# Optimization experiments

Measured on AMD Instinct MI355X. Metric: run time of the kernel, lower is better.

Reference implementation:

```python
import jax, jax.numpy as jnp
import numpy as np

TEMPERATURE = 0.5
TAU_PLUS = 0.1
EPS = 1e-8


def setup_inputs() -> dict:
    key = jax.random.key(0)
    k1, k2 = jax.random.split(key)
    B, D = 8192, 128
    z_i = jax.random.normal(k1, (B, D), dtype=jnp.float32)
    z_j = jax.random.normal(k2, (B, D), dtype=jnp.float32)
    return {"z_i": z_i, "z_j": z_j}


def _l2_normalize(x, axis=1, eps=1e-12):
    # matches torch F.normalize: x / max(||x||, eps)
    n = jnp.linalg.norm(x, axis=axis, keepdims=True)
    return x / jnp.maximum(n, eps)


def reference(z_i, z_j):
    B = z_i.shape[0]
    zi = _l2_normalize(z_i, axis=1)
    zj = _l2_normalize(z_j, axis=1)
    reps = jnp.concatenate([zi, zj], axis=0)  # [2B, D]
    sim = jnp.matmul(reps, reps.T) / TEMPERATURE  # [2B, 2B]
    sim = sim - jnp.max(sim, axis=1, keepdims=True)
    mask = jnp.eye(2 * B, dtype=bool)
    sim = jnp.where(mask, -9e15, sim)
    pos = jnp.exp(jnp.sum(zi * zj, axis=-1) / TEMPERATURE)  # [B]
    positives = jnp.concatenate([pos, pos], axis=0)  # [2B]
    neg_sum = jnp.sum(jnp.exp(sim), axis=1)  # [2B]
    Ng = (-TAU_PLUS * B * positives + neg_sum) / (1.0 - TAU_PLUS)
    Ng = jnp.maximum(Ng, B * jnp.exp(jnp.asarray(-1.0 / TEMPERATURE, dtype=sim.dtype)))
    loss = -jnp.log(positives / (positives + Ng + EPS))
    return jnp.mean(loss)
```

## Files before the change

### kernel.cpp

```cpp
#include <hip/hip_runtime.h>
#include <hip/hip_bf16.h>

typedef __attribute__((ext_vector_type(8))) short bf16x8;
typedef __attribute__((ext_vector_type(4))) float f32x4;

#define B_ROWS 8192
#define NROWS 16384
#define D 128
#define C1 2.8853900817779268f
#define E_M2 0.13533528323661270f
#define RSCALE 1.6986436f
#define TILE_COLS 64
#define TILE_BYTES (TILE_COLS * D * 2)
#define NSPLIT 16
#define NBLK (64 * NSPLIT)
#define NSLICE 8

__device__ __forceinline__ float fast_exp2(float x) {
#if __has_builtin(__builtin_amdgcn_exp2f)
    return __builtin_amdgcn_exp2f(x);
#else
    float r; asm("v_exp_f32 %0, %1" : "=v"(r) : "v"(x)); return r;
#endif
}
__device__ __forceinline__ float fast_log2(float x) {
#if __has_builtin(__builtin_amdgcn_logf)
    return __builtin_amdgcn_logf(x);
#else
    float r; asm("v_log_f32 %0, %1" : "=v"(r) : "v"(x)); return r;
#endif
}

__device__ __forceinline__ unsigned short f2bf(float f) {
    union { float f; unsigned u; } v; v.f = f;
    unsigned r = v.u + 0x7FFFu + ((v.u >> 16) & 1u);
    return (unsigned short)(r >> 16);
}

__device__ __host__ __forceinline__ int colpart_off(int I) {
    return I * NROWS - 128 * I * (I + 1);
}

__global__ __launch_bounds__(256) void k_norm(const float* __restrict__ zi,
                                              const float* __restrict__ zj,
                                              unsigned* __restrict__ repsU,
                                              float* __restrict__ pos) {
    int w = threadIdx.x >> 6, lane = threadIdx.x & 63;
    int row = blockIdx.x * 4 + w;
    const float2* a2 = (const float2*)(zi + (size_t)row * D);
    const float2* b2 = (const float2*)(zj + (size_t)row * D);
    float2 a = a2[lane], b = b2[lane];
    float si = a.x * a.x + a.y * a.y;
    float sj = b.x * b.x + b.y * b.y;
    float sd = a.x * b.x + a.y * b.y;
#pragma unroll
    for (int m = 32; m; m >>= 1) {
        si += __shfl_xor(si, m);
        sj += __shfl_xor(sj, m);
        sd += __shfl_xor(sd, m);
    }
    float inv_i = 1.0f / fmaxf(sqrtf(si), 1e-12f);
    float inv_j = 1.0f / fmaxf(sqrtf(sj), 1e-12f);
    float sa = inv_i * RSCALE, sb = inv_j * RSCALE;
    repsU[(size_t)row * 64 + lane] =
        (unsigned)f2bf(a.x * sa) | ((unsigned)f2bf(a.y * sa) << 16);
    repsU[(size_t)(row + B_ROWS) * 64 + lane] =
        (unsigned)f2bf(b.x * sb) | ((unsigned)f2bf(b.y * sb) << 16);
    if (lane == 0) pos[row] = fast_exp2(sd * inv_i * inv_j * C1);
}

__global__ __launch_bounds__(256, 2) void k_negsum(const unsigned short* __restrict__ R,
                                                   float* __restrict__ rowpart,
                                                   float* __restrict__ colpart) {
    __shared__ char smem[2][TILE_BYTES];
    __shared__ float colacc[2][4][4][80];
    int I = blockIdx.x >> 4;
    int s = blockIdx.x & (NSPLIT - 1);
    int rowBase = I << 8;
    int dph = (s - ((I << 2) & 15)) & 15;
    int jstart = (I << 2) + dph;
    int nt = (jstart < 256) ? (((255 - jstart) >> 4) + 1) : 0;

    int w = threadIdx.x >> 6;
    int lane = threadIdx.x & 63;
    int lr = lane & 15, lk = lane >> 4;
    int waveRow = rowBase + w * 64;

    bf16x8 afrag[4][4];
#pragma unroll
    for (int r = 0; r < 4; ++r)
#pragma unroll
        for (int kk = 0; kk < 4; ++kk)
            afrag[r][kk] = *(const bf16x8*)(R + (size_t)(waveRow + r * 16 + lr) * D + kk * 32 + lk * 8);

    int srcoff[4], dstoff[4];
#pragma unroll
    for (int j = 0; j < 4; ++j) {
        int o = (w * 4 + j) * 1024 + lane * 16;
        int row = o >> 8, c = o & 255;
        srcoff[j] = row * 256 + (c ^ ((row & 7) << 4));
        dstoff[j] = (w * 4 + j) * 1024;
    }

    const char* Rb = (const char*)R;

    int m64 = (lr & 4) << 4;
    int lbase = lr * 256 + ((lk * 16) ^ ((lr & 3) << 4));

    float acc[4][4] = {};

#define STAGE(buf, jj)                                                            \
    do {                                                                          \
        const char* tb_ = Rb + (size_t)(jj) * (TILE_COLS * 256);                  \
        _Pragma("unroll")                                                         \
        for (int j = 0; j < 4; ++j)                                               \
            __builtin_amdgcn_global_load_lds(                                     \
                (const __attribute__((address_space(1))) unsigned*)(tb_ + srcoff[j]), \
                (__attribute__((address_space(3))) unsigned*)(&smem[buf][dstoff[j]]), \
                16, 0, 0);                                                        \
    } while (0)

#define BATCH_BODY(DIAG)                                                          \
    do {                                                                          \
        _Pragma("unroll")                                                         \
        for (int ct = 0; ct < 4; ++ct) {                                          \
            _Pragma("unroll")                                                     \
            for (int r = 0; r < 4; ++r) {                                         \
                f32x4 c = {0.f, 0.f, 0.f, 0.f};                                   \
                c = __builtin_amdgcn_mfma_f32_16x16x32_bf16(afrag[r][0], bf[ct][0], c, 0, 0, 0); \
                c = __builtin_amdgcn_mfma_f32_16x16x32_bf16(afrag[r][1], bf[ct][1], c, 0, 0, 0); \
                c = __builtin_amdgcn_mfma_f32_16x16x32_bf16(afrag[r][2], bf[ct][2], c, 0, 0, 0); \
                c = __builtin_amdgcn_mfma_f32_16x16x32_bf16(afrag[r][3], bf[ct][3], c, 0, 0, 0); \
                if (DIAG && ct == r) {                                            \
                    _Pragma("unroll")                                             \
                    for (int q = 0; q < 4; ++q)                                   \
                        if (lk * 4 + q != lr) {                                   \
                            float e = fast_exp2(c[q]);                            \
                            acc[r][q] += e; csum[ct] += e;                        \
                        }                                                         \
                } else {                                                          \
                    _Pragma("unroll")                                             \
                    for (int q = 0; q < 4; ++q) {                                 \
                        float e = fast_exp2(c[q]);                                \
                        acc[r][q] += e; csum[ct] += e;                            \
                    }                                                             \
                }                                                                 \
            }                                                                     \
        }                                                                         \
    } while (0)

    if (nt > 0) STAGE(0, jstart);
    __syncthreads();
    int cur = 0;
    for (int t = 0; t < nt; ++t) {
        int jt = jstart + (t << 4);
        int colBase = jt << 6;
        if (t > 0 && w == ((t + 3) & 3)) {
            int pcb = colBase - 1024;
            if (pcb >= rowBase + 256) {
                int par = (t - 1) & 1;
                float v = 0.f;
#pragma unroll
                for (int u = 0; u < 16; ++u) v += colacc[par][u >> 2][u & 3][lane];
                colpart[colpart_off(I) + pcb + lane - ((I + 1) << 8)] = v;
            }
        }
        if (t + 1 < nt) STAGE(cur ^ 1, jt + 16);
        const char* sb = &smem[cur][0] + lbase;
        bf16x8 bf[4][4];
#pragma unroll
        for (int ct = 0; ct < 4; ++ct)
#pragma unroll
            for (int kk = 0; kk < 4; ++kk)
                bf[ct][kk] = *(const bf16x8*)(sb + ct * 4096 + ((kk * 64) ^ m64));
        float csum[4] = {0.f, 0.f, 0.f, 0.f};
        bool offdiag = (colBase >= rowBase + 256);
        if (colBase == waveRow) {
            BATCH_BODY(true);
        } else {
            BATCH_BODY(false);
        }
        if (offdiag) {
            int par = t & 1;
#pragma unroll
            for (int ct = 0; ct < 4; ++ct)
                colacc[par][w][lk][ct * 16 + lr] = csum[ct];
        }
        __syncthreads();
        cur ^= 1;
    }
    if (nt > 0 && w == ((nt + 3) & 3)) {
        int pcb = (jstart + ((nt - 1) << 4)) << 6;
        if (pcb >= rowBase + 256) {
            int par = (nt - 1) & 1;
            float v = 0.f;
#pragma unroll
            for (int u = 0; u < 16; ++u) v += colacc[par][u >> 2][u & 3][lane];
            colpart[colpart_off(I) + pcb + lane - ((I + 1) << 8)] = v;
        }
    }
#undef STAGE
#undef BATCH_BODY

#pragma unroll
    for (int r = 0; r < 4; ++r)
#pragma unroll
        for (int q = 0; q < 4; ++q) {
            float v = acc[r][q];
            v += __shfl_xor(v, 1);
            v += __shfl_xor(v, 2);
            v += __shfl_xor(v, 4);
            v += __shfl_xor(v, 8);
            if (lr == 0)
                rowpart[(size_t)s * NROWS + waveRow + r * 16 + lk * 4 + q] = v;
        }
}

__global__ __launch_bounds__(256) void k_negred(const float* __restrict__ rowpart,
                                                const float* __restrict__ colpart,
                                                float* __restrict__ negp) {
    int g = blockIdx.x >> 3;
    int z = blockIdx.x & (NSLICE - 1);
    int i = g * 256 + threadIdx.x;
    float a = 0.f;
#pragma unroll
    for (int s = z; s < NSPLIT; s += NSLICE)
        a += rowpart[(size_t)s * NROWS + i];
    for (int I = z; I < g; I += NSLICE)
        a += colpart[colpart_off(I) + i - ((I + 1) << 8)];
    negp[(size_t)z * NROWS + i] = a;
}

__global__ __launch_bounds__(256) void k_loss1(const float* __restrict__ pos,
                                               const float* __restrict__ negp,
                                               float* __restrict__ bsum) {
    int i = blockIdx.x * 256 + threadIdx.x;
    float neg = 0.f;
#pragma unroll
    for (int z = 0; z < NSLICE; ++z) neg += negp[(size_t)z * NROWS + i];
    neg *= E_M2;
    float p = pos[i & (B_ROWS - 1)];
    float Ng = fmaxf((neg - 819.2f * p) * (1.0f / 0.9f), 8192.0f * E_M2);
    float l = fast_log2((p + Ng + 1e-8f) / p) * 0.69314718056f;
#pragma unroll
    for (int m = 32; m; m >>= 1) l += __shfl_xor(l, m);
    __shared__ float s4[4];
    int wv = threadIdx.x >> 6;
    if ((threadIdx.x & 63) == 0) s4[wv] = l;
    __syncthreads();
    if (threadIdx.x == 0) bsum[blockIdx.x] = s4[0] + s4[1] + s4[2] + s4[3];
}

__global__ void k_loss2(const float* __restrict__ bsum, float* __restrict__ out) {
    float v = bsum[threadIdx.x];
#pragma unroll
    for (int m = 32; m; m >>= 1) v += __shfl_xor(v, m);
    if (threadIdx.x == 0) out[0] = v * (1.0f / (float)NROWS);
}

extern "C" void kernel_launch(void* const* d_in, const int* in_sizes, int n_in,
                              void* d_out, int out_size, void* d_ws, size_t ws_size,
                              hipStream_t stream) {
    const float* zi = (const float*)d_in[0];
    const float* zj = (const float*)d_in[1];
    char* ws = (char*)d_ws;
    unsigned short* reps = (unsigned short*)ws;
    float* pos = (float*)(ws + 4194304);
    float* rowpart = pos + B_ROWS;
    float* colpart = rowpart + (size_t)NSPLIT * NROWS;
    float* negp = colpart + 516096;
    float* bsum = negp + (size_t)NSLICE * NROWS;
    float* out = (float*)d_out;

    k_norm<<<B_ROWS / 4, 256, 0, stream>>>(zi, zj, (unsigned*)reps, pos);
    k_negsum<<<NBLK, 256, 0, stream>>>(reps, rowpart, colpart);
    k_negred<<<64 * NSLICE, 256, 0, stream>>>(rowpart, colpart, negp);
    k_loss1<<<NROWS / 256, 256, 0, stream>>>(pos, negp, bsum);
    k_loss2<<<1, 64, 0, stream>>>(bsum, out);
}
```

Measured before the change: 65.93 us.

## Use per-wave triple-buffered LDS ring with vmcnt waits, no block barriers

Replaces the block-wide double-buffered 64-column tile staging with a per-wave three-slot LDS ring of 16-column subtiles. Each wave loads its own copy of the subtiles via global_load_lds and waits on vmcnt, so the per-tile __syncthreads is gone. Column partial sums are kept in a per-wave LDS array and reduced once after the loop. In exchange every wave now fetches the full column stream itself (4x the global/L2 traffic), LDS use rises, and the launch-bounds occupancy hint of 2 is dropped.

Measured after the change: 82.51 us. 1.25x slower.

```diff
diff --git a/kernel.cpp b/kernel.cpp
--- a/kernel.cpp
+++ b/kernel.cpp
@@ -10,8 +10,6 @@
 #define C1 2.8853900817779268f
 #define E_M2 0.13533528323661270f
 #define RSCALE 1.6986436f
-#define TILE_COLS 64
-#define TILE_BYTES (TILE_COLS * D * 2)
 #define NSPLIT 16
 #define NBLK (64 * NSPLIT)
 #define NSLICE 8
@@ -69,22 +67,24 @@
     if (lane == 0) pos[row] = fast_exp2(sd * inv_i * inv_j * C1);
 }
 
-__global__ __launch_bounds__(256, 2) void k_negsum(const unsigned short* __restrict__ R,
-                                                   float* __restrict__ rowpart,
-                                                   float* __restrict__ colpart) {
-    __shared__ char smem[2][TILE_BYTES];
-    __shared__ float colacc[2][4][4][80];
+__global__ __launch_bounds__(256) void k_negsum(const unsigned short* __restrict__ R,
+                                                float* __restrict__ rowpart,
+                                                float* __restrict__ colpart) {
+    __shared__ char ring[4][3][4096];
+    __shared__ float scratch[4][64];
+    __shared__ float colaccL[4][64][16];
     int I = blockIdx.x >> 4;
     int s = blockIdx.x & (NSPLIT - 1);
     int rowBase = I << 8;
     int dph = (s - ((I << 2) & 15)) & 15;
     int jstart = (I << 2) + dph;
     int nt = (jstart < 256) ? (((255 - jstart) >> 4) + 1) : 0;
+    int n = nt << 2;
 
     int w = threadIdx.x >> 6;
     int lane = threadIdx.x & 63;
     int lr = lane & 15, lk = lane >> 4;
-    int waveRow = rowBase + w * 64;
+    int waveRow = rowBase + (w << 6);
 
     bf16x8 afrag[4][4];
 #pragma unroll
@@ -93,15 +93,13 @@
         for (int kk = 0; kk < 4; ++kk)
             afrag[r][kk] = *(const bf16x8*)(R + (size_t)(waveRow + r * 16 + lr) * D + kk * 32 + lk * 8);
 
-    int srcoff[4], dstoff[4];
+    int srcoff[4];
 #pragma unroll
     for (int j = 0; j < 4; ++j) {
-        int o = (w * 4 + j) * 1024 + lane * 16;
+        int o = j * 1024 + lane * 16;
         int row = o >> 8, c = o & 255;
         srcoff[j] = row * 256 + (c ^ ((row & 7) << 4));
-        dstoff[j] = (w * 4 + j) * 1024;
-    }
-
+    }
     const char* Rb = (const char*)R;
 
     int m64 = (lr & 4) << 4;
@@ -109,98 +107,97 @@
 
     float acc[4][4] = {};
 
-#define STAGE(buf, jj)                                                            \
+#define STAGE16(u, slot)                                                          \
     do {                                                                          \
-        const char* tb_ = Rb + (size_t)(jj) * (TILE_COLS * 256);                  \
+        const char* tb_ = Rb + (size_t)jstart * 16384 +                           \
+                          (size_t)((u) >> 2) * 262144 + (size_t)((u) & 3) * 4096; \
         _Pragma("unroll")                                                         \
         for (int j = 0; j < 4; ++j)                                               \
             __builtin_amdgcn_global_load_lds(                                     \
                 (const __attribute__((address_space(1))) unsigned*)(tb_ + srcoff[j]), \
-                (__attribute__((address_space(3))) unsigned*)(&smem[buf][dstoff[j]]), \
+                (__attribute__((address_space(3))) unsigned*)(&ring[w][slot][j * 1024]), \
                 16, 0, 0);                                                        \
     } while (0)
 
-#define BATCH_BODY(DIAG)                                                          \
-    do {                                                                          \
-        _Pragma("unroll")                                                         \
-        for (int ct = 0; ct < 4; ++ct) {                                          \
-            _Pragma("unroll")                                                     \
-            for (int r = 0; r < 4; ++r) {                                         \
-                f32x4 c = {0.f, 0.f, 0.f, 0.f};                                   \
-                c = __builtin_amdgcn_mfma_f32_16x16x32_bf16(afrag[r][0], bf[ct][0], c, 0, 0, 0); \
-                c = __builtin_amdgcn_mfma_f32_16x16x32_bf16(afrag[r][1], bf[ct][1], c, 0, 0, 0); \
-                c = __builtin_amdgcn_mfma_f32_16x16x32_bf16(afrag[r][2], bf[ct][2], c, 0, 0, 0); \
-                c = __builtin_amdgcn_mfma_f32_16x16x32_bf16(afrag[r][3], bf[ct][3], c, 0, 0, 0); \
-                if (DIAG && ct == r) {                                            \
-                    _Pragma("unroll")                                             \
-                    for (int q = 0; q < 4; ++q)                                   \
-                        if (lk * 4 + q != lr) {                                   \
-                            float e = fast_exp2(c[q]);                            \
-                            acc[r][q] += e; csum[ct] += e;                        \
-                        }                                                         \
-                } else {                                                          \
-                    _Pragma("unroll")                                             \
-                    for (int q = 0; q < 4; ++q) {                                 \
-                        float e = fast_exp2(c[q]);                                \
-                        acc[r][q] += e; csum[ct] += e;                            \
-                    }                                                             \
-                }                                                                 \
-            }                                                                     \
-        }                                                                         \
-    } while (0)
-
-    if (nt > 0) STAGE(0, jstart);
+    if (n > 0) STAGE16(0, 0);
+    if (n > 1) STAGE16(1, 1);
+    int csl = 0;
+    for (int u = 0; u < n; ++u) {
+        int rem = n - 1 - u;
+        if (rem >= 2) {
+            int stslot = (csl == 0) ? 2 : csl - 1;
+            STAGE16(u + 2, stslot);
+            asm volatile("s_waitcnt vmcnt(8)" ::: "memory");
+        } else if (rem == 1) {
+            asm volatile("s_waitcnt vmcnt(4)" ::: "memory");
+        } else {
+            asm volatile("s_waitcnt vmcnt(0)" ::: "memory");
+        }
+        const char* sb = &ring[w][csl][0] + lbase;
+        bf16x8 bf[4];
+#pragma unroll
+        for (int kk = 0; kk < 4; ++kk)
+            bf[kk] = *(const bf16x8*)(sb + ((kk * 64) ^ m64));
+        int c0 = jstart * 64 + ((u >> 2) << 10) + ((u & 3) << 4);
+        float csum = 0.f;
+        bool dg = (unsigned)(c0 - waveRow) < 64u;
+        if (dg) {
+            int rd = (c0 - waveRow) >> 4;
+#pragma unroll
+            for (int r = 0; r < 4; ++r) {
+                f32x4 c = {0.f, 0.f, 0.f, 0.f};
+                c = __builtin_amdgcn_mfma_f32_16x16x32_bf16(afrag[r][0], bf[0], c, 0, 0, 0);
+                c = __builtin_amdgcn_mfma_f32_16x16x32_bf16(afrag[r][1], bf[1], c, 0, 0, 0);
+                c = __builtin_amdgcn_mfma_f32_16x16x32_bf16(afrag[r][2], bf[2], c, 0, 0, 0);
+                c = __builtin_amdgcn_mfma_f32_16x16x32_bf16(afrag[r][3], bf[3], c, 0, 0, 0);
+                if (r == rd) {
+#pragma unroll
+                    for (int q = 0; q < 4; ++q)
+                        if (lk * 4 + q != lr) {
+                            float e = fast_exp2(c[q]);
+                            acc[r][q] += e; csum += e;
+                        }
+                } else {
+#pragma unroll
+                    for (int q = 0; q < 4; ++q) {
+                        float e = fast_exp2(c[q]);
+                        acc[r][q] += e; csum += e;
+                    }
+                }
+            }
+        } else {
+#pragma unroll
+            for (int r = 0; r < 4; ++r) {
+                f32x4 c = {0.f, 0.f, 0.f, 0.f};
+                c = __builtin_amdgcn_mfma_f32_16x16x32_bf16(afrag[r][0], bf[0], c, 0, 0, 0);
+                c = __builtin_amdgcn_mfma_f32_16x16x32_bf16(afrag[r][1], bf[1], c, 0, 0, 0);
+                c = __builtin_amdgcn_mfma_f32_16x16x32_bf16(afrag[r][2], bf[2], c, 0, 0, 0);
+                c = __builtin_amdgcn_mfma_f32_16x16x32_bf16(afrag[r][3], bf[3], c, 0, 0, 0);
+#pragma unroll
+                for (int q = 0; q < 4; ++q) {
+                    float e = fast_exp2(c[q]);
+                    acc[r][q] += e; csum += e;
+                }
+            }
+        }
+        scratch[w][lane] = csum;
+        float v = scratch[w][lr] + scratch[w][lr + 16] +
+                  scratch[w][lr + 32] + scratch[w][lr + 48];
+        if (lk == 0) colaccL[w][u][lr] = v;
+        csl = (csl == 2) ? 0 : csl + 1;
+    }
+#undef STAGE16
+
     __syncthreads();
-    int cur = 0;
-    for (int t = 0; t < nt; ++t) {
-        int jt = jstart + (t << 4);
-        int colBase = jt << 6;
-        if (t > 0 && w == ((t + 3) & 3)) {
-            int pcb = colBase - 1024;
-            if (pcb >= rowBase + 256) {
-                int par = (t - 1) & 1;
-                float v = 0.f;
-#pragma unroll
-                for (int u = 0; u < 16; ++u) v += colacc[par][u >> 2][u & 3][lane];
-                colpart[colpart_off(I) + pcb + lane - ((I + 1) << 8)] = v;
-            }
-        }
-        if (t + 1 < nt) STAGE(cur ^ 1, jt + 16);
-        const char* sb = &smem[cur][0] + lbase;
-        bf16x8 bf[4][4];
-#pragma unroll
-        for (int ct = 0; ct < 4; ++ct)
-#pragma unroll
-            for (int kk = 0; kk < 4; ++kk)
-                bf[ct][kk] = *(const bf16x8*)(sb + ct * 4096 + ((kk * 64) ^ m64));
-        float csum[4] = {0.f, 0.f, 0.f, 0.f};
-        bool offdiag = (colBase >= rowBase + 256);
-        if (colBase == waveRow) {
-            BATCH_BODY(true);
-        } else {
-            BATCH_BODY(false);
-        }
-        if (offdiag) {
-            int par = t & 1;
-#pragma unroll
-            for (int ct = 0; ct < 4; ++ct)
-                colacc[par][w][lk][ct * 16 + lr] = csum[ct];
-        }
-        __syncthreads();
-        cur ^= 1;
-    }
-    if (nt > 0 && w == ((nt + 3) & 3)) {
-        int pcb = (jstart + ((nt - 1) << 4)) << 6;
-        if (pcb >= rowBase + 256) {
-            int par = (nt - 1) & 1;
-            float v = 0.f;
-#pragma unroll
-            for (int u = 0; u < 16; ++u) v += colacc[par][u >> 2][u & 3][lane];
-            colpart[colpart_off(I) + pcb + lane - ((I + 1) << 8)] = v;
-        }
-    }
-#undef STAGE
-#undef BATCH_BODY
+    for (int pid = threadIdx.x; pid < (n << 4); pid += 256) {
+        int u = pid >> 4, cl = pid & 15;
+        int c0 = jstart * 64 + ((u >> 2) << 10) + ((u & 3) << 4);
+        if (c0 >= rowBase + 256) {
+            float v = colaccL[0][u][cl] + colaccL[1][u][cl] +
+                      colaccL[2][u][cl] + colaccL[3][u][cl];
+            colpart[colpart_off(I) + c0 + cl - ((I + 1) << 8)] = v;
+        }
+    }
 
 #pragma unroll
     for (int r = 0; r < 4; ++r)
```
